# Kernel optimization log

Hardware: AMD Instinct MI355X
Metric: run time of the kernel (lower is better)

## Reference

```python
import jax, jax.numpy as jnp
import numpy as np

N_NODES = 50000
N_EDGES = 800000
IN_FEATS = 128
HID = 32
HEADS = 8
OUT_FEATS = 32
NEG_SLOPE = 0.2


def gat_conv(x, W, a_l, a_r, b, src, dst, n):
    """DGL-style GATConv. x:[n,Din], W:[Din,H*C], a_l/a_r:[H,C], b:[H*C]. Returns [n,H,C]."""
    H, C = a_l.shape
    ft = (x @ W).reshape(n, H, C)                      # projected features
    el = jnp.einsum('nhc,hc->nh', ft, a_l)             # [n,H]
    er = jnp.einsum('nhc,hc->nh', ft, a_r)             # [n,H]
    e = jax.nn.leaky_relu(el[src] + er[dst], NEG_SLOPE)  # [E,H] edge logits
    # edge softmax per destination node (numerically stable)
    m = jax.lax.stop_gradient(jax.ops.segment_max(e, dst, num_segments=n))
    ex = jnp.exp(e - m[dst])
    s = jax.ops.segment_sum(ex, dst, num_segments=n)
    alpha = ex / s[dst]                                # [E,H]
    out = jax.ops.segment_sum(alpha[:, :, None] * ft[src], dst, num_segments=n)
    return out + b.reshape(1, H, C)


def setup_inputs() -> dict:
    key = jax.random.key(0)
    ks = jax.random.split(key, 16)
    p = lambda k, shape: (jax.random.normal(k, shape, dtype=jnp.float32) * 0.1)
    d0, d1 = IN_FEATS, HID * HEADS
    return {
        'x': jax.random.normal(ks[0], (N_NODES, IN_FEATS), dtype=jnp.float32),
        'src': jax.random.randint(ks[1], (N_EDGES,), 0, N_NODES, dtype=jnp.int32),
        'dst': jax.random.randint(ks[2], (N_EDGES,), 0, N_NODES, dtype=jnp.int32),
        'W0': p(ks[3], (d0, HEADS * HID)), 'al0': p(ks[4], (HEADS, HID)), 'ar0': p(ks[5], (HEADS, HID)), 'b0': jnp.zeros((HEADS * HID,), jnp.float32),
        'W1': p(ks[6], (d1, HEADS * HID)), 'al1': p(ks[7], (HEADS, HID)), 'ar1': p(ks[8], (HEADS, HID)), 'b1': jnp.zeros((HEADS * HID,), jnp.float32),
        'W2': p(ks[9], (d1, 1 * OUT_FEATS)), 'al2': p(ks[10], (1, OUT_FEATS)), 'ar2': p(ks[11], (1, OUT_FEATS)), 'b2': jnp.zeros((OUT_FEATS,), jnp.float32),
    }


def reference(x, src, dst, W0, al0, ar0, b0, W1, al1, ar1, b1, W2, al2, ar2, b2):
    n = x.shape[0]
    h = gat_conv(x, W0, al0, ar0, b0, src, dst, n)
    h = jax.nn.relu(h.reshape(n, -1))                  # concat heads + ReLU
    h = gat_conv(h, W1, al1, ar1, b1, src, dst, n)
    h = jax.nn.relu(h.reshape(n, -1))
    h = gat_conv(h, W2, al2, ar2, b2, src, dst, n)
    h = jax.nn.relu(h.reshape(n, -1))                  # loop applies relu after every layer
    # squeeze() on [n, out_feats] is a no-op here; softmax over classes
    return jax.nn.softmax(h, axis=1)
```

## Files before the change

kernel.cpp:

```cpp
#include <hip/hip_runtime.h>
#include <hip/hip_fp16.h>
#include <cstdint>
#include <cstddef>


#define IN_FEATS 128

typedef _Float16 f16x8 __attribute__((ext_vector_type(8)));
typedef float f32x4 __attribute__((ext_vector_type(4)));

__device__ __forceinline__ unsigned char f32_to_fp8(float f) {
    int p = __builtin_amdgcn_cvt_pk_fp8_f32(f, 0.f, 0, false);
    return (unsigned char)(p & 0xff);
}
__device__ __forceinline__ void fp8x4_to_f32(unsigned w, float* o) {
    o[0] = __builtin_amdgcn_cvt_f32_fp8(w, 0);
    o[1] = __builtin_amdgcn_cvt_f32_fp8(w, 1);
    o[2] = __builtin_amdgcn_cvt_f32_fp8(w, 2);
    o[3] = __builtin_amdgcn_cvt_f32_fp8(w, 3);
}

__global__ __launch_bounds__(256) void k_prep(
    const float* __restrict__ W0, const float* __restrict__ W1, const float* __restrict__ W2,
    const float* __restrict__ al0, const float* __restrict__ ar0,
    const float* __restrict__ al1, const float* __restrict__ ar1,
    const float* __restrict__ al2, const float* __restrict__ ar2,
    _Float16* __restrict__ W0T, _Float16* __restrict__ W1T, _Float16* __restrict__ W2T,
    _Float16* __restrict__ WLR0, _Float16* __restrict__ WLR1, _Float16* __restrict__ WLR2) {
    int bid = blockIdx.x, t = threadIdx.x;
    if (bid < 128) {
        int i = bid * 256 + t;
        int nn = i >> 7, kk = i & 127;
        W0T[i] = (_Float16)W0[(size_t)kk * 256 + nn];
    } else if (bid < 384) {
        int i = (bid - 128) * 256 + t;
        int nn = i >> 8, kk = i & 255;
        W1T[i] = (_Float16)W1[(size_t)kk * 256 + nn];
    } else if (bid < 416) {
        int i = (bid - 384) * 256 + t;
        int nn = i >> 8, kk = i & 255;
        W2T[i] = (_Float16)W2[(size_t)kk * 32 + nn];
    } else if (bid < 424) {
        int i = (bid - 416) * 256 + t;
        int j = i >> 7, k = i & 127;
        int h = j & 7;
        const float* av = (j < 8) ? al0 : ar0;
        float sum = 0.f;
        #pragma unroll 8
        for (int c = 0; c < 32; ++c) sum += W0[(size_t)k * 256 + h * 32 + c] * av[h * 32 + c];
        WLR0[i] = (_Float16)sum;
    } else if (bid < 440) {
        int i = (bid - 424) * 256 + t;
        int j = i >> 8, k = i & 255;
        int h = j & 7;
        const float* av = (j < 8) ? al1 : ar1;
        float sum = 0.f;
        #pragma unroll 8
        for (int c = 0; c < 32; ++c) sum += W1[(size_t)k * 256 + h * 32 + c] * av[h * 32 + c];
        WLR1[i] = (_Float16)sum;
    } else {
        int i = (bid - 440) * 256 + t;
        int j = i >> 8, k = i & 255;
        float sum = 0.f;
        if (j < 2) {
            const float* av = (j == 0) ? al2 : ar2;
            #pragma unroll 8
            for (int c = 0; c < 32; ++c) sum += W2[(size_t)k * 32 + c] * av[c];
        }
        WLR2[i] = (_Float16)sum;
    }
}

template <int K, typename AT>
__global__ __launch_bounds__(256) void k_mfma_gemm(const AT* __restrict__ A,
                                                   const _Float16* __restrict__ BT,
                                                   const _Float16* __restrict__ WLRT,
                                                   unsigned char* __restrict__ C8,
                                                   float* __restrict__ el,
                                                   float* __restrict__ er, int M) {
    const int N = 256;
    const int LDA = K + 8;
    __shared__ _Float16 As[64 * LDA];
    int tid = threadIdx.x;
    int lane = tid & 63, wc = tid >> 6;
    int mr = blockIdx.x * 64;
    #pragma unroll
    for (int it = 0; it < K / 32; ++it) {
        int idx = (it * 256 + tid) * 8;
        int row = idx / K, col = idx % K;
        int rowg = mr + row; if (rowg > M - 1) rowg = M - 1;
        f16x8 v;
        if constexpr (sizeof(AT) == 2) {
            v = *(const f16x8*)(A + (size_t)rowg * K + col);
        } else {
            float4 u0 = *(const float4*)(A + (size_t)rowg * K + col);
            float4 u1 = *(const float4*)(A + (size_t)rowg * K + col + 4);
            v[0] = (_Float16)u0.x; v[1] = (_Float16)u0.y;
            v[2] = (_Float16)u0.z; v[3] = (_Float16)u0.w;
            v[4] = (_Float16)u1.x; v[5] = (_Float16)u1.y;
            v[6] = (_Float16)u1.z; v[7] = (_Float16)u1.w;
        }
        *(f16x8*)(As + row * LDA + col) = v;
    }
    __syncthreads();
    const _Float16* pb[4];
    #pragma unroll
    for (int j = 0; j < 4; ++j) {
        int col = wc * 64 + j * 16 + (lane & 15);
        pb[j] = BT + (size_t)col * K + (lane >> 4) * 8;
    }
    const _Float16* pe = WLRT + (size_t)(lane & 15) * K + (lane >> 4) * 8;
    const _Float16* pa = As + (lane & 15) * LDA + (lane >> 4) * 8;
    f32x4 acc[4][4] = {};
    f32x4 acce[4] = {};
    #pragma unroll
    for (int k0 = 0; k0 < K; k0 += 32) {
        f16x8 a[4], b[4];
        #pragma unroll
        for (int t = 0; t < 4; ++t) a[t] = *(const f16x8*)(pa + t * 16 * LDA + k0);
        #pragma unroll
        for (int t = 0; t < 4; ++t) b[t] = *(const f16x8*)(pb[t] + k0);
        #pragma unroll
        for (int i = 0; i < 4; ++i)
            #pragma unroll
            for (int j = 0; j < 4; ++j)
                acc[i][j] = __builtin_amdgcn_mfma_f32_16x16x32_f16(a[i], b[j], acc[i][j], 0, 0, 0);
        if (wc == 3) {
            f16x8 be = *(const f16x8*)(pe + k0);
            #pragma unroll
            for (int i = 0; i < 4; ++i)
                acce[i] = __builtin_amdgcn_mfma_f32_16x16x32_f16(a[i], be, acce[i], 0, 0, 0);
        }
    }
    #pragma unroll
    for (int i = 0; i < 4; ++i)
        #pragma unroll
        for (int j = 0; j < 4; ++j)
            #pragma unroll
            for (int r = 0; r < 4; ++r) {
                int row = mr + i * 16 + (lane >> 4) * 4 + r;
                int col = wc * 64 + j * 16 + (lane & 15);
                if (row < M) C8[(size_t)row * N + col] = f32_to_fp8(acc[i][j][r]);
            }
    if (wc == 3) {
        int c16 = lane & 15;
        #pragma unroll
        for (int i = 0; i < 4; ++i)
            #pragma unroll
            for (int r = 0; r < 4; ++r) {
                int row = mr + i * 16 + (lane >> 4) * 4 + r;
                if (row < M) {
                    if (c16 < 8) el[row * 8 + c16] = acce[i][r];
                    else         er[row * 8 + (c16 - 8)] = acce[i][r];
                }
            }
    }
}

template <int K>
__global__ __launch_bounds__(256) void k_mfma_gemm32(const _Float16* __restrict__ A,
                                                     const _Float16* __restrict__ BT,
                                                     const _Float16* __restrict__ WLRT,
                                                     _Float16* __restrict__ C,
                                                     float* __restrict__ el,
                                                     float* __restrict__ er, int M) {
    const int N = 32;
    int lane = threadIdx.x & 63, w = threadIdx.x >> 6;
    int mr = blockIdx.x * 256 + w * 64;
    const _Float16* pa[4];
    const _Float16* pb[2];
    #pragma unroll
    for (int t = 0; t < 4; ++t) {
        int row = mr + t * 16 + (lane & 15);
        if (row > M - 1) row = M - 1;
        pa[t] = A + (size_t)row * K + (lane >> 4) * 8;
    }
    #pragma unroll
    for (int t = 0; t < 2; ++t) {
        int col = t * 16 + (lane & 15);
        pb[t] = BT + (size_t)col * K + (lane >> 4) * 8;
    }
    const _Float16* pe = WLRT + (size_t)(lane & 15) * K + (lane >> 4) * 8;
    f32x4 acc[4][2] = {};
    f32x4 acce[4] = {};
    #pragma unroll
    for (int k0 = 0; k0 < K; k0 += 32) {
        f16x8 a[4], b[2], be;
        #pragma unroll
        for (int t = 0; t < 4; ++t) a[t] = *(const f16x8*)(pa[t] + k0);
        #pragma unroll
        for (int t = 0; t < 2; ++t) b[t] = *(const f16x8*)(pb[t] + k0);
        be = *(const f16x8*)(pe + k0);
        #pragma unroll
        for (int i = 0; i < 4; ++i) {
            #pragma unroll
            for (int j = 0; j < 2; ++j)
                acc[i][j] = __builtin_amdgcn_mfma_f32_16x16x32_f16(a[i], b[j], acc[i][j], 0, 0, 0);
            acce[i] = __builtin_amdgcn_mfma_f32_16x16x32_f16(a[i], be, acce[i], 0, 0, 0);
        }
    }
    int c16 = lane & 15;
    #pragma unroll
    for (int i = 0; i < 4; ++i)
        #pragma unroll
        for (int r = 0; r < 4; ++r) {
            int row = mr + i * 16 + (lane >> 4) * 4 + r;
            if (row < M) {
                #pragma unroll
                for (int j = 0; j < 2; ++j)
                    C[(size_t)row * N + j * 16 + c16] = (_Float16)acc[i][j][r];
                if (c16 == 0) el[row] = acce[i][r];
                else if (c16 == 1) er[row] = acce[i][r];
            }
        }
}

__global__ void k_deg(const int* __restrict__ dst, int* __restrict__ deg, int E) {
    int e = blockIdx.x * blockDim.x + threadIdx.x;
    if (e < E) atomicAdd(deg + dst[e], 1);
}
__global__ __launch_bounds__(256) void k_scan1(const int* __restrict__ deg,
                                               int* __restrict__ bsum, int n) {
    int base = blockIdx.x * 1024;
    int t = threadIdx.x;
    int s = 0;
    #pragma unroll
    for (int i = 0; i < 4; ++i) {
        int idx = base + t * 4 + i;
        if (idx < n) s += deg[idx];
    }
    __shared__ int red[256];
    red[t] = s; __syncthreads();
    for (int off = 128; off; off >>= 1) {
        if (t < off) red[t] += red[t + off];
        __syncthreads();
    }
    if (t == 0) bsum[blockIdx.x] = red[0];
}
__global__ __launch_bounds__(256) void k_scan3(const int* __restrict__ deg,
                                               const int* __restrict__ bsum,
                                               int* __restrict__ row_ptr, int n, int E) {
    int base = blockIdx.x * 1024;
    int t = threadIdx.x;
    __shared__ int boff;
    if (t == 0) {
        int s = 0;
        for (int j = 0; j < blockIdx.x; ++j) s += bsum[j];
        boff = s;
        if (blockIdx.x == 0) row_ptr[n] = E;
    }
    int loc[4]; int s = 0;
    #pragma unroll
    for (int i = 0; i < 4; ++i) {
        int idx = base + t * 4 + i;
        loc[i] = (idx < n) ? deg[idx] : 0;
        s += loc[i];
    }
    __shared__ int part[256];
    part[t] = s; __syncthreads();
    for (int off = 1; off < 256; off <<= 1) {
        int v = (t >= off) ? part[t - off] : 0;
        __syncthreads();
        part[t] += v;
        __syncthreads();
    }
    int run = boff + part[t] - s;
    #pragma unroll
    for (int i = 0; i < 4; ++i) {
        int idx = base + t * 4 + i;
        if (idx < n) row_ptr[idx] = run;
        run += loc[i];
    }
}
__global__ void k_fill(const int* __restrict__ dst, const int* __restrict__ src,
                       const int* __restrict__ row_ptr,
                       int* __restrict__ fill, int* __restrict__ csrc, int E) {
    int e = blockIdx.x * blockDim.x + threadIdx.x;
    if (e < E) {
        int d = dst[e];
        int pos = row_ptr[d] + atomicAdd(fill + d, 1);
        csrc[pos] = src[e];
    }
}

__global__ __launch_bounds__(256) void k_fused256(const int* __restrict__ row_ptr,
                                                  const int* __restrict__ csrc,
                                                  const float* __restrict__ el,
                                                  const float* __restrict__ er,
                                                  const unsigned char* __restrict__ ft8,
                                                  const float* __restrict__ b,
                                                  _Float16* __restrict__ out, int n) {
    int wave = threadIdx.x >> 6;
    int lane = threadIdx.x & 63;
    int v = blockIdx.x * 4 + wave;
    if (v >= n) return;
    int g = lane >> 4;
    int l16 = lane & 15;
    int h = l16 >> 1;
    float erv = er[v * 8 + h];
    const float* elh = el + h;
    int e0 = row_ptr[v], e1 = row_ptr[v + 1];
    float s = 0.f;
    float a[16] = {};
    int k = e0 + g;
    for (; k + 4 < e1; k += 8) {
        int sn0 = csrc[k];
        int sn1 = csrc[k + 4];
        float ev0 = elh[sn0 * 8] + erv;
        float ev1 = elh[sn1 * 8] + erv;
        ev0 = ev0 > 0.f ? ev0 : 0.2f * ev0;
        ev1 = ev1 > 0.f ? ev1 : 0.2f * ev1;
        float w0 = __expf(ev0);
        float w1 = __expf(ev1);
        uint4 q0 = *(const uint4*)(ft8 + ((size_t)sn0 << 8) + l16 * 16);
        uint4 q1 = *(const uint4*)(ft8 + ((size_t)sn1 << 8) + l16 * 16);
        float f0[16], f1[16];
        fp8x4_to_f32(q0.x, f0);     fp8x4_to_f32(q0.y, f0 + 4);
        fp8x4_to_f32(q0.z, f0 + 8); fp8x4_to_f32(q0.w, f0 + 12);
        fp8x4_to_f32(q1.x, f1);     fp8x4_to_f32(q1.y, f1 + 4);
        fp8x4_to_f32(q1.z, f1 + 8); fp8x4_to_f32(q1.w, f1 + 12);
        s += w0 + w1;
        #pragma unroll
        for (int j = 0; j < 16; ++j) a[j] += w0 * f0[j];
        #pragma unroll
        for (int j = 0; j < 16; ++j) a[j] += w1 * f1[j];
    }
    if (k < e1) {
        int sn = csrc[k];
        float ev = elh[sn * 8] + erv;
        ev = ev > 0.f ? ev : 0.2f * ev;
        float w = __expf(ev);
        s += w;
        uint4 q = *(const uint4*)(ft8 + ((size_t)sn << 8) + l16 * 16);
        float f[16];
        fp8x4_to_f32(q.x, f);     fp8x4_to_f32(q.y, f + 4);
        fp8x4_to_f32(q.z, f + 8); fp8x4_to_f32(q.w, f + 12);
        #pragma unroll
        for (int j = 0; j < 16; ++j) a[j] += w * f[j];
    }
    s += __shfl_xor(s, 16, 64);
    s += __shfl_xor(s, 32, 64);
    #pragma unroll
    for (int j = 0; j < 16; ++j) {
        a[j] += __shfl_xor(a[j], 16, 64);
        a[j] += __shfl_xor(a[j], 32, 64);
    }
    if (g == 0) {
        float inv = s > 0.f ? 1.f / s : 0.f;
        const float* bp = b + l16 * 16;
        f16x8 o0, o1;
        #pragma unroll
        for (int j = 0; j < 8; ++j) o0[j] = (_Float16)fmaxf(a[j] * inv + bp[j], 0.f);
        #pragma unroll
        for (int j = 0; j < 8; ++j) o1[j] = (_Float16)fmaxf(a[8 + j] * inv + bp[8 + j], 0.f);
        _Float16* op = out + ((size_t)v << 8) + l16 * 16;
        *(f16x8*)op = o0;
        *(f16x8*)(op + 8) = o1;
    }
}

__global__ __launch_bounds__(256) void k_fused_out(const int* __restrict__ row_ptr,
                                                   const int* __restrict__ csrc,
                                                   const float* __restrict__ el,
                                                   const float* __restrict__ er,
                                                   const _Float16* __restrict__ ft,
                                                   const float* __restrict__ b,
                                                   float* __restrict__ out, int n) {
    int v = blockIdx.x * 16 + (threadIdx.x >> 4);
    int sub = threadIdx.x & 15;
    int g = sub >> 2;
    int l4 = sub & 3;
    if (v >= n) return;
    float erv = er[v];
    int e0 = row_ptr[v], e1 = row_ptr[v + 1];
    float s = 0.f;
    float a[8] = {};
    for (int k = e0 + g; k < e1; k += 4) {
        int sn = csrc[k];
        float ev = el[sn] + erv;
        ev = ev > 0.f ? ev : 0.2f * ev;
        float w = __expf(ev);
        s += w;
        f16x8 f = *(const f16x8*)(ft + (sn << 5) + l4 * 8);
        #pragma unroll
        for (int j = 0; j < 8; ++j) a[j] += w * (float)f[j];
    }
    s += __shfl_xor(s, 4, 64);
    s += __shfl_xor(s, 8, 64);
    #pragma unroll
    for (int j = 0; j < 8; ++j) {
        a[j] += __shfl_xor(a[j], 4, 64);
        a[j] += __shfl_xor(a[j], 8, 64);
    }
    float inv = s > 0.f ? 1.f / s : 0.f;
    const float* bp = b + l4 * 8;
    float val[8];
    float mx = -INFINITY;
    #pragma unroll
    for (int j = 0; j < 8; ++j) {
        val[j] = fmaxf(a[j] * inv + bp[j], 0.f);
        mx = fmaxf(mx, val[j]);
    }
    mx = fmaxf(mx, __shfl_xor(mx, 1, 64));
    mx = fmaxf(mx, __shfl_xor(mx, 2, 64));
    float ex[8];
    float sum = 0.f;
    #pragma unroll
    for (int j = 0; j < 8; ++j) { ex[j] = __expf(val[j] - mx); sum += ex[j]; }
    sum += __shfl_xor(sum, 1, 64);
    sum += __shfl_xor(sum, 2, 64);
    float isum = 1.f / sum;
    if (g == 0) {
        float* op = out + ((size_t)v << 5) + l4 * 8;
        *(float4*)op = make_float4(ex[0] * isum, ex[1] * isum, ex[2] * isum, ex[3] * isum);
        *(float4*)(op + 4) = make_float4(ex[4] * isum, ex[5] * isum, ex[6] * isum, ex[7] * isum);
    }
}

extern "C" void kernel_launch(void* const* d_in, const int* in_sizes, int n_in,
                              void* d_out, int out_size, void* d_ws, size_t ws_size,
                              hipStream_t stream) {
    const float* x  = (const float*)d_in[0];
    const int* src  = (const int*)d_in[1];
    const int* dst  = (const int*)d_in[2];
    const float* W0 = (const float*)d_in[3];
    const float* al0 = (const float*)d_in[4];
    const float* ar0 = (const float*)d_in[5];
    const float* b0  = (const float*)d_in[6];
    const float* W1 = (const float*)d_in[7];
    const float* al1 = (const float*)d_in[8];
    const float* ar1 = (const float*)d_in[9];
    const float* b1  = (const float*)d_in[10];
    const float* W2 = (const float*)d_in[11];
    const float* al2 = (const float*)d_in[12];
    const float* ar2 = (const float*)d_in[13];
    const float* b2  = (const float*)d_in[14];
    float* out = (float*)d_out;

    const int n = in_sizes[0] / IN_FEATS;
    const int E = in_sizes[1];

    char* p = (char*)d_ws;
    auto alloc = [&](size_t bytes) {
        void* r = (void*)p;
        p += (bytes + 255) & ~(size_t)255;
        return r;
    };
    unsigned char* ft8 = (unsigned char*)alloc((size_t)n * 256);
    _Float16* h16   = (_Float16*)alloc((size_t)n * 256 * 2);
    _Float16* ft16  = (_Float16*)alloc((size_t)n * 32 * 2);
    _Float16* W0T   = (_Float16*)alloc((size_t)256 * 128 * 2);
    _Float16* W1T   = (_Float16*)alloc((size_t)256 * 256 * 2);
    _Float16* W2T   = (_Float16*)alloc((size_t)32 * 256 * 2);
    _Float16* WLR0  = (_Float16*)alloc((size_t)16 * 128 * 2);
    _Float16* WLR1  = (_Float16*)alloc((size_t)16 * 256 * 2);
    _Float16* WLR2  = (_Float16*)alloc((size_t)16 * 256 * 2);
    float* el       = (float*)alloc((size_t)n * 8 * 4);
    float* er       = (float*)alloc((size_t)n * 8 * 4);
    int* deg        = (int*)alloc((size_t)n * 4);
    int* fill       = (int*)alloc((size_t)n * 4);
    int* row_ptr    = (int*)alloc((size_t)(n + 1) * 4);
    int* csrc       = (int*)alloc((size_t)E * 4);
    int* bsum       = (int*)alloc((size_t)64 * 4);

    const int EB = (E + 255) / 256;
    const int NBCH = (n + 1023) / 1024;

    hipMemsetAsync(deg, 0, (size_t)((char*)fill - (char*)deg) + (size_t)n * 4, stream);
    k_deg<<<EB, 256, 0, stream>>>(dst, deg, E);
    k_scan1<<<NBCH, 256, 0, stream>>>(deg, bsum, n);
    k_scan3<<<NBCH, 256, 0, stream>>>(deg, bsum, row_ptr, n, E);
    k_fill<<<EB, 256, 0, stream>>>(dst, src, row_ptr, fill, csrc, E);

    k_prep<<<456, 256, 0, stream>>>(W0, W1, W2, al0, ar0, al1, ar1, al2, ar2,
                                    W0T, W1T, W2T, WLR0, WLR1, WLR2);

    const int GB = (n + 63) / 64;
    const int GB32 = (n + 255) / 256;
    const int FB = (n + 3) / 4;
    const int OB = (n + 15) / 16;

    k_mfma_gemm<128, float><<<GB, 256, 0, stream>>>(x, W0T, WLR0, ft8, el, er, n);
    k_fused256<<<FB, 256, 0, stream>>>(row_ptr, csrc, el, er, ft8, b0, h16, n);

    k_mfma_gemm<256, _Float16><<<GB, 256, 0, stream>>>(h16, W1T, WLR1, ft8, el, er, n);
    k_fused256<<<FB, 256, 0, stream>>>(row_ptr, csrc, el, er, ft8, b1, h16, n);

    k_mfma_gemm32<256><<<GB32, 256, 0, stream>>>(h16, W2T, WLR2, ft16, el, er, n);
    k_fused_out<<<OB, 256, 0, stream>>>(row_ptr, csrc, el, er, ft16, b2, out, n);
}
```

Before: 337.2 us.

## Merge degree count into prep kernel and CSR fill into layer-0 GEMM

The degree-counting atomics now run as extra blocks of the weight-prep kernel, and the CSR fill runs as extra blocks of a dedicated layer-0 GEMM kernel. This removes two kernel launches and lets independent work overlap on the GPU. The edge aggregation loop is also unrolled from 2 to 4 edges, with all feature loads issued before the math to increase memory-level parallelism. The cost is higher register pressure in the aggregation kernel and a duplicated GEMM body for layer 0.

```diff
diff --git a/kernel.cpp b/kernel.cpp
--- a/kernel.cpp
+++ b/kernel.cpp
@@ -20,14 +20,20 @@
     o[3] = __builtin_amdgcn_cvt_f32_fp8(w, 3);
 }
 
-__global__ __launch_bounds__(256) void k_prep(
+__global__ __launch_bounds__(256) void k_degprep(
     const float* __restrict__ W0, const float* __restrict__ W1, const float* __restrict__ W2,
     const float* __restrict__ al0, const float* __restrict__ ar0,
     const float* __restrict__ al1, const float* __restrict__ ar1,
     const float* __restrict__ al2, const float* __restrict__ ar2,
     _Float16* __restrict__ W0T, _Float16* __restrict__ W1T, _Float16* __restrict__ W2T,
-    _Float16* __restrict__ WLR0, _Float16* __restrict__ WLR1, _Float16* __restrict__ WLR2) {
+    _Float16* __restrict__ WLR0, _Float16* __restrict__ WLR1, _Float16* __restrict__ WLR2,
+    const int* __restrict__ dst, int* __restrict__ deg, int E) {
     int bid = blockIdx.x, t = threadIdx.x;
+    if (bid >= 456) {
+        int e = (bid - 456) * 256 + t;
+        if (e < E) atomicAdd(deg + dst[e], 1);
+        return;
+    }
     if (bid < 128) {
         int i = bid * 256 + t;
         int nn = i >> 7, kk = i & 127;
@@ -58,7 +64,7 @@
         #pragma unroll 8
         for (int c = 0; c < 32; ++c) sum += W1[(size_t)k * 256 + h * 32 + c] * av[h * 32 + c];
         WLR1[i] = (_Float16)sum;
-    } else {
+    } else if (bid < 456) {
         int i = (bid - 440) * 256 + t;
         int j = i >> 8, k = i & 255;
         float sum = 0.f;
@@ -71,8 +77,98 @@
     }
 }
 
-template <int K, typename AT>
-__global__ __launch_bounds__(256) void k_mfma_gemm(const AT* __restrict__ A,
+__global__ __launch_bounds__(256) void k_gemm0_fill(
+    const float* __restrict__ A, const _Float16* __restrict__ BT,
+    const _Float16* __restrict__ WLRT, unsigned char* __restrict__ C8,
+    float* __restrict__ el, float* __restrict__ er, int M, int GB,
+    const int* __restrict__ dst, const int* __restrict__ src,
+    const int* __restrict__ row_ptr, int* __restrict__ fill,
+    int* __restrict__ csrc, int E) {
+    const int K = 128, N = 256, LDA = K + 8;
+    __shared__ _Float16 As[64 * LDA];
+    int tid = threadIdx.x;
+    if ((int)blockIdx.x >= GB) {
+        int e = ((int)blockIdx.x - GB) * 256 + tid;
+        if (e < E) {
+            int d = dst[e];
+            int pos = row_ptr[d] + atomicAdd(fill + d, 1);
+            csrc[pos] = src[e];
+        }
+        return;
+    }
+    int lane = tid & 63, wc = tid >> 6;
+    int mr = blockIdx.x * 64;
+    #pragma unroll
+    for (int it = 0; it < K / 32; ++it) {
+        int idx = (it * 256 + tid) * 8;
+        int row = idx / K, col = idx % K;
+        int rowg = mr + row; if (rowg > M - 1) rowg = M - 1;
+        float4 u0 = *(const float4*)(A + (size_t)rowg * K + col);
+        float4 u1 = *(const float4*)(A + (size_t)rowg * K + col + 4);
+        f16x8 v;
+        v[0] = (_Float16)u0.x; v[1] = (_Float16)u0.y;
+        v[2] = (_Float16)u0.z; v[3] = (_Float16)u0.w;
+        v[4] = (_Float16)u1.x; v[5] = (_Float16)u1.y;
+        v[6] = (_Float16)u1.z; v[7] = (_Float16)u1.w;
+        *(f16x8*)(As + row * LDA + col) = v;
+    }
+    __syncthreads();
+    const _Float16* pb[4];
+    #pragma unroll
+    for (int j = 0; j < 4; ++j) {
+        int col = wc * 64 + j * 16 + (lane & 15);
+        pb[j] = BT + (size_t)col * K + (lane >> 4) * 8;
+    }
+    const _Float16* pe = WLRT + (size_t)(lane & 15) * K + (lane >> 4) * 8;
+    const _Float16* pa = As + (lane & 15) * LDA + (lane >> 4) * 8;
+    f32x4 acc[4][4] = {};
+    f32x4 acce[4] = {};
+    #pragma unroll
+    for (int k0 = 0; k0 < K; k0 += 32) {
+        f16x8 a[4], b[4];
+        #pragma unroll
+        for (int t = 0; t < 4; ++t) a[t] = *(const f16x8*)(pa + t * 16 * LDA + k0);
+        #pragma unroll
+        for (int t = 0; t < 4; ++t) b[t] = *(const f16x8*)(pb[t] + k0);
+        #pragma unroll
+        for (int i = 0; i < 4; ++i)
+            #pragma unroll
+            for (int j = 0; j < 4; ++j)
+                acc[i][j] = __builtin_amdgcn_mfma_f32_16x16x32_f16(a[i], b[j], acc[i][j], 0, 0, 0);
+        if (wc == 3) {
+            f16x8 be = *(const f16x8*)(pe + k0);
+            #pragma unroll
+            for (int i = 0; i < 4; ++i)
+                acce[i] = __builtin_amdgcn_mfma_f32_16x16x32_f16(a[i], be, acce[i], 0, 0, 0);
+        }
+    }
+    #pragma unroll
+    for (int i = 0; i < 4; ++i)
+        #pragma unroll
+        for (int j = 0; j < 4; ++j)
+            #pragma unroll
+            for (int r = 0; r < 4; ++r) {
+                int row = mr + i * 16 + (lane >> 4) * 4 + r;
+                int col = wc * 64 + j * 16 + (lane & 15);
+                if (row < M) C8[(size_t)row * N + col] = f32_to_fp8(acc[i][j][r]);
+            }
+    if (wc == 3) {
+        int c16 = lane & 15;
+        #pragma unroll
+        for (int i = 0; i < 4; ++i)
+            #pragma unroll
+            for (int r = 0; r < 4; ++r) {
+                int row = mr + i * 16 + (lane >> 4) * 4 + r;
+                if (row < M) {
+                    if (c16 < 8) el[row * 8 + c16] = acce[i][r];
+                    else         er[row * 8 + (c16 - 8)] = acce[i][r];
+                }
+            }
+    }
+}
+
+template <int K>
+__global__ __launch_bounds__(256) void k_mfma_gemm(const _Float16* __restrict__ A,
                                                    const _Float16* __restrict__ BT,
                                                    const _Float16* __restrict__ WLRT,
                                                    unsigned char* __restrict__ C8,
@@ -89,17 +185,7 @@
         int idx = (it * 256 + tid) * 8;
         int row = idx / K, col = idx % K;
         int rowg = mr + row; if (rowg > M - 1) rowg = M - 1;
-        f16x8 v;
-        if constexpr (sizeof(AT) == 2) {
-            v = *(const f16x8*)(A + (size_t)rowg * K + col);
-        } else {
-            float4 u0 = *(const float4*)(A + (size_t)rowg * K + col);
-            float4 u1 = *(const float4*)(A + (size_t)rowg * K + col + 4);
-            v[0] = (_Float16)u0.x; v[1] = (_Float16)u0.y;
-            v[2] = (_Float16)u0.z; v[3] = (_Float16)u0.w;
-            v[4] = (_Float16)u1.x; v[5] = (_Float16)u1.y;
-            v[6] = (_Float16)u1.z; v[7] = (_Float16)u1.w;
-        }
+        f16x8 v = *(const f16x8*)(A + (size_t)rowg * K + col);
         *(f16x8*)(As + row * LDA + col) = v;
     }
     __syncthreads();
@@ -215,10 +301,6 @@
         }
 }
 
-__global__ void k_deg(const int* __restrict__ dst, int* __restrict__ deg, int E) {
-    int e = blockIdx.x * blockDim.x + threadIdx.x;
-    if (e < E) atomicAdd(deg + dst[e], 1);
-}
 __global__ __launch_bounds__(256) void k_scan1(const int* __restrict__ deg,
                                                int* __restrict__ bsum, int n) {
     int base = blockIdx.x * 1024;
@@ -270,16 +352,6 @@
         int idx = base + t * 4 + i;
         if (idx < n) row_ptr[idx] = run;
         run += loc[i];
-    }
-}
-__global__ void k_fill(const int* __restrict__ dst, const int* __restrict__ src,
-                       const int* __restrict__ row_ptr,
-                       int* __restrict__ fill, int* __restrict__ csrc, int E) {
-    int e = blockIdx.x * blockDim.x + threadIdx.x;
-    if (e < E) {
-        int d = dst[e];
-        int pos = row_ptr[d] + atomicAdd(fill + d, 1);
-        csrc[pos] = src[e];
     }
 }
 
@@ -303,29 +375,44 @@
     float s = 0.f;
     float a[16] = {};
     int k = e0 + g;
-    for (; k + 4 < e1; k += 8) {
+    for (; k + 12 < e1; k += 16) {
         int sn0 = csrc[k];
         int sn1 = csrc[k + 4];
+        int sn2 = csrc[k + 8];
+        int sn3 = csrc[k + 12];
         float ev0 = elh[sn0 * 8] + erv;
         float ev1 = elh[sn1 * 8] + erv;
+        float ev2 = elh[sn2 * 8] + erv;
+        float ev3 = elh[sn3 * 8] + erv;
+        uint4 q0 = *(const uint4*)(ft8 + ((size_t)sn0 << 8) + l16 * 16);
+        uint4 q1 = *(const uint4*)(ft8 + ((size_t)sn1 << 8) + l16 * 16);
+        uint4 q2 = *(const uint4*)(ft8 + ((size_t)sn2 << 8) + l16 * 16);
+        uint4 q3 = *(const uint4*)(ft8 + ((size_t)sn3 << 8) + l16 * 16);
         ev0 = ev0 > 0.f ? ev0 : 0.2f * ev0;
         ev1 = ev1 > 0.f ? ev1 : 0.2f * ev1;
-        float w0 = __expf(ev0);
-        float w1 = __expf(ev1);
-        uint4 q0 = *(const uint4*)(ft8 + ((size_t)sn0 << 8) + l16 * 16);
-        uint4 q1 = *(const uint4*)(ft8 + ((size_t)sn1 << 8) + l16 * 16);
-        float f0[16], f1[16];
-        fp8x4_to_f32(q0.x, f0);     fp8x4_to_f32(q0.y, f0 + 4);
-        fp8x4_to_f32(q0.z, f0 + 8); fp8x4_to_f32(q0.w, f0 + 12);
-        fp8x4_to_f32(q1.x, f1);     fp8x4_to_f32(q1.y, f1 + 4);
-        fp8x4_to_f32(q1.z, f1 + 8); fp8x4_to_f32(q1.w, f1 + 12);
-        s += w0 + w1;
-        #pragma unroll
-        for (int j = 0; j < 16; ++j) a[j] += w0 * f0[j];
-        #pragma unroll
-        for (int j = 0; j < 16; ++j) a[j] += w1 * f1[j];
-    }
-    if (k < e1) {
+        ev2 = ev2 > 0.f ? ev2 : 0.2f * ev2;
+        ev3 = ev3 > 0.f ? ev3 : 0.2f * ev3;
+        float w0 = __expf(ev0), w1 = __expf(ev1), w2 = __expf(ev2), w3 = __expf(ev3);
+        s += (w0 + w1) + (w2 + w3);
+        float f[16];
+        fp8x4_to_f32(q0.x, f);     fp8x4_to_f32(q0.y, f + 4);
+        fp8x4_to_f32(q0.z, f + 8); fp8x4_to_f32(q0.w, f + 12);
+        #pragma unroll
+        for (int j = 0; j < 16; ++j) a[j] += w0 * f[j];
+        fp8x4_to_f32(q1.x, f);     fp8x4_to_f32(q1.y, f + 4);
+        fp8x4_to_f32(q1.z, f + 8); fp8x4_to_f32(q1.w, f + 12);
+        #pragma unroll
+        for (int j = 0; j < 16; ++j) a[j] += w1 * f[j];
+        fp8x4_to_f32(q2.x, f);     fp8x4_to_f32(q2.y, f + 4);
+        fp8x4_to_f32(q2.z, f + 8); fp8x4_to_f32(q2.w, f + 12);
+        #pragma unroll
+        for (int j = 0; j < 16; ++j) a[j] += w2 * f[j];
+        fp8x4_to_f32(q3.x, f);     fp8x4_to_f32(q3.y, f + 4);
+        fp8x4_to_f32(q3.z, f + 8); fp8x4_to_f32(q3.w, f + 12);
+        #pragma unroll
+        for (int j = 0; j < 16; ++j) a[j] += w3 * f[j];
+    }
+    for (; k < e1; k += 4) {
         int sn = csrc[k];
         float ev = elh[sn * 8] + erv;
         ev = ev > 0.f ? ev : 0.2f * ev;
@@ -465,25 +552,24 @@
 
     const int EB = (E + 255) / 256;
     const int NBCH = (n + 1023) / 1024;
-
-    hipMemsetAsync(deg, 0, (size_t)((char*)fill - (char*)deg) + (size_t)n * 4, stream);
-    k_deg<<<EB, 256, 0, stream>>>(dst, deg, E);
-    k_scan1<<<NBCH, 256, 0, stream>>>(deg, bsum, n);
-    k_scan3<<<NBCH, 256, 0, stream>>>(deg, bsum, row_ptr, n, E);
-    k_fill<<<EB, 256, 0, stream>>>(dst, src, row_ptr, fill, csrc, E);
-
-    k_prep<<<456, 256, 0, stream>>>(W0, W1, W2, al0, ar0, al1, ar1, al2, ar2,
-                                    W0T, W1T, W2T, WLR0, WLR1, WLR2);
-
     const int GB = (n + 63) / 64;
     const int GB32 = (n + 255) / 256;
     const int FB = (n + 3) / 4;
     const int OB = (n + 15) / 16;
 
-    k_mfma_gemm<128, float><<<GB, 256, 0, stream>>>(x, W0T, WLR0, ft8, el, er, n);
+    hipMemsetAsync(deg, 0, (size_t)((char*)fill - (char*)deg) + (size_t)n * 4, stream);
+
+    k_degprep<<<456 + EB, 256, 0, stream>>>(W0, W1, W2, al0, ar0, al1, ar1, al2, ar2,
+                                            W0T, W1T, W2T, WLR0, WLR1, WLR2,
+                                            dst, deg, E);
+    k_scan1<<<NBCH, 256, 0, stream>>>(deg, bsum, n);
+    k_scan3<<<NBCH, 256, 0, stream>>>(deg, bsum, row_ptr, n, E);
+
+    k_gemm0_fill<<<GB + EB, 256, 0, stream>>>(x, W0T, WLR0, ft8, el, er, n, GB,
+                                              dst, src, row_ptr, fill, csrc, E);
     k_fused256<<<FB, 256, 0, stream>>>(row_ptr, csrc, el, er, ft8, b0, h16, n);
 
-    k_mfma_gemm<256, _Float16><<<GB, 256, 0, stream>>>(h16, W1T, WLR1, ft8, el, er, n);
+    k_mfma_gemm<256><<<GB, 256, 0, stream>>>(h16, W1T, WLR1, ft8, el, er, n);
     k_fused256<<<FB, 256, 0, stream>>>(row_ptr, csrc, el, er, ft8, b1, h16, n);
 
     k_mfma_gemm32<256><<<GB32, 256, 0, stream>>>(h16, W2T, WLR2, ft16, el, er, n);
```

Measured after the change: 323.1 us. -4.2%, faster.
